# Optimization experiments

Measured on AMD Instinct MI355X. Metric: run time of the kernel, lower is better.

## Reference

```python
import jax, jax.numpy as jnp
import numpy as np
from jax import lax

IMG = 800.0      # image size (square)
STRIDE = 8       # FPN P3 stride
HF = 100; WF = 100; C = 256
A = 3            # anchors per location (aspect ratios 0.5,1,2)
PRE_NMS = 2000   # rpn_pre_nms_top_n_train
POST_NMS = 1000  # rpn_post_nms_top_n_test
NMS_TH = 0.7     # rpn_nms_thresh
POOL = 7; SR = 2 # ROIAlign output size / sampling ratio
NUM_CLASSES = 2
REP = 1024       # TwoMLPHead representation size
BBOX_CLAMP = float(np.log(1000.0 / 16.0))


def make_anchors():
    size = 64.0
    ratios = np.array([0.5, 1.0, 2.0])
    h = size * np.sqrt(ratios); w = size / np.sqrt(ratios)
    base = np.stack([-w / 2, -h / 2, w / 2, h / 2], 1)  # [A,4]
    sy = np.arange(HF) * STRIDE; sx = np.arange(WF) * STRIDE
    yy, xx = np.meshgrid(sy, sx, indexing='ij')
    shifts = np.stack([xx, yy, xx, yy], -1).reshape(-1, 1, 4)  # [H*W,1,4]
    return (shifts + base[None]).reshape(-1, 4).astype(np.float32)  # [H*W*A,4], (H,W,A) order


def conv2d(x, w, b, pad):
    y = lax.conv_general_dilated(x, w, (1, 1), pad, dimension_numbers=('NCHW', 'OIHW', 'NCHW'))
    return y + b[None, :, None, None]


def decode(deltas, anchors):
    wa = anchors[:, 2] - anchors[:, 0]; ha = anchors[:, 3] - anchors[:, 1]
    cxa = anchors[:, 0] + 0.5 * wa; cya = anchors[:, 1] + 0.5 * ha
    dw = jnp.minimum(deltas[:, 2], BBOX_CLAMP)
    dh = jnp.minimum(deltas[:, 3], BBOX_CLAMP)
    cx = deltas[:, 0] * wa + cxa; cy = deltas[:, 1] * ha + cya
    w = jnp.exp(dw) * wa; h = jnp.exp(dh) * ha
    return jnp.stack([cx - 0.5 * w, cy - 0.5 * h, cx + 0.5 * w, cy + 0.5 * h], 1)


def box_iou_one(box, boxes):
    lt = jnp.maximum(box[:2], boxes[:, :2]); rb = jnp.minimum(box[2:], boxes[:, 2:])
    wh = jnp.clip(rb - lt, 0.0)
    inter = wh[:, 0] * wh[:, 1]
    a1 = (box[2] - box[0]) * (box[3] - box[1])
    a2 = (boxes[:, 2] - boxes[:, 0]) * (boxes[:, 3] - boxes[:, 1])
    return inter / (a1 + a2 - inter + 1e-9)


def nms_fixed(boxes, scores, thresh, keep_n):
    order = jnp.argsort(-scores)
    b = boxes[order]; s = scores[order]
    n = b.shape[0]; ar = jnp.arange(n)
    def body(i, alive):
        sup = (box_iou_one(b[i], b) > thresh) & (ar > i) & alive[i]
        return alive & (~sup)
    alive = lax.fori_loop(0, n, body, jnp.ones((n,), bool))
    _, idx = lax.top_k(jnp.where(alive, s, -jnp.inf), keep_n)
    return b[idx]  # [keep_n,4]


def roi_align_one(feat, roi):
    # feat [C,Hf,Wf], roi [4] in image coords (x1,y1,x2,y2)
    Hf, Wf = feat.shape[1], feat.shape[2]
    x1, y1, x2, y2 = roi / STRIDE
    bw = (x2 - x1) / POOL; bh = (y2 - y1) / POOL
    k = (jnp.arange(POOL * SR) + 0.5) / SR  # [S]
    xs = jnp.clip(x1 + bw * k, 0.0, Wf - 1.0)
    ys = jnp.clip(y1 + bh * k, 0.0, Hf - 1.0)
    y0 = jnp.floor(ys); x0 = jnp.floor(xs)
    y0i = y0.astype(jnp.int32); x0i = x0.astype(jnp.int32)
    y1i = jnp.minimum(y0i + 1, Hf - 1); x1i = jnp.minimum(x0i + 1, Wf - 1)
    ly = ys - y0; lx = xs - x0; hy = 1.0 - ly; hx = 1.0 - lx
    v00 = feat[:, y0i[:, None], x0i[None, :]]
    v01 = feat[:, y0i[:, None], x1i[None, :]]
    v10 = feat[:, y1i[:, None], x0i[None, :]]
    v11 = feat[:, y1i[:, None], x1i[None, :]]
    out = ((hy[:, None] * hx[None, :]) * v00 + (hy[:, None] * lx[None, :]) * v01
           + (ly[:, None] * hx[None, :]) * v10 + (ly[:, None] * lx[None, :]) * v11)  # [C,S,S]
    return out.reshape(feat.shape[0], POOL, SR, POOL, SR).mean(axis=(2, 4))  # [C,7,7]


def _forward(features, rpn_conv_w, rpn_conv_b, rpn_cls_w, rpn_cls_b, rpn_bbox_w, rpn_bbox_b,
             fc1_w, fc1_b, fc2_w, fc2_b, cls_w, cls_b, reg_w, reg_b):
    B = features.shape[0]
    t = jax.nn.relu(conv2d(features, rpn_conv_w, rpn_conv_b, 'SAME'))
    obj = conv2d(t, rpn_cls_w, rpn_cls_b, 'VALID').transpose(0, 2, 3, 1).reshape(B, -1)  # (H,W,A)
    dl = (conv2d(t, rpn_bbox_w, rpn_bbox_b, 'VALID')
          .reshape(B, A, 4, HF, WF).transpose(0, 3, 4, 1, 2).reshape(B, -1, 4))
    anchors = jnp.asarray(make_anchors())

    def per_image(feat, o, d):
        s, idx = lax.top_k(o, PRE_NMS)
        boxes = jnp.clip(decode(d[idx], anchors[idx]), 0.0, IMG)
        rois = nms_fixed(boxes, s, NMS_TH, POST_NMS)
        return jax.vmap(lambda r: roi_align_one(feat, r))(rois)  # [K,C,7,7]

    pooled = jax.vmap(per_image)(features, obj, dl)  # [B,K,C,7,7]
    x = pooled.reshape(B, POST_NMS, -1)
    x = jax.nn.relu(x @ fc1_w + fc1_b)
    x = jax.nn.relu(x @ fc2_w + fc2_b)
    return jnp.concatenate([x @ cls_w + cls_b, x @ reg_w + reg_b], axis=-1)  # [B,K,10]


def setup_inputs() -> dict:
    key = jax.random.key(0)
    ks = jax.random.split(key, 8)
    def w(k, shape, s=0.01):
        return jax.random.normal(k, shape, jnp.float32) * s
    return {
        'features': jax.random.normal(ks[0], (2, C, HF, WF), jnp.float32),
        'rpn_conv_w': w(ks[1], (C, C, 3, 3)), 'rpn_conv_b': jnp.zeros((C,), jnp.float32),
        'rpn_cls_w': w(ks[2], (A, C, 1, 1)), 'rpn_cls_b': jnp.zeros((A,), jnp.float32),
        'rpn_bbox_w': w(ks[3], (4 * A, C, 1, 1)), 'rpn_bbox_b': jnp.zeros((4 * A,), jnp.float32),
        'fc1_w': w(ks[4], (C * POOL * POOL, REP)), 'fc1_b': jnp.zeros((REP,), jnp.float32),
        'fc2_w': w(ks[5], (REP, REP)), 'fc2_b': jnp.zeros((REP,), jnp.float32),
        'cls_w': w(ks[6], (REP, NUM_CLASSES)), 'cls_b': jnp.zeros((NUM_CLASSES,), jnp.float32),
        'reg_w': w(ks[7], (REP, 4 * NUM_CLASSES)), 'reg_b': jnp.zeros((4 * NUM_CLASSES,), jnp.float32),
    }


def reference(features, rpn_conv_w, rpn_conv_b, rpn_cls_w, rpn_cls_b, rpn_bbox_w, rpn_bbox_b,
              fc1_w, fc1_b, fc2_w, fc2_b, cls_w, cls_b, reg_w, reg_b):
    return _forward(features, rpn_conv_w, rpn_conv_b, rpn_cls_w, rpn_cls_b, rpn_bbox_w,
                    rpn_bbox_b, fc1_w, fc1_b, fc2_w, fc2_b, cls_w, cls_b, reg_w, reg_b)
```

## Files before the change

### kernel.cpp

```cpp
#include <hip/hip_runtime.h>
#include <hip/hip_bf16.h>
#include <math.h>

#define NPOS 10000
#define NANCH 30000
#define PRE 2000
#define POST 1000
#define RESQ 4096
#define CLAMPD 4.135166556742356
#define FPH 102
#define FPW 132

typedef __attribute__((ext_vector_type(8))) short bf16x8v;
typedef __attribute__((ext_vector_type(4))) float f32x4v;

__device__ __forceinline__ unsigned long long mapu64(double f) {
  unsigned long long b = (unsigned long long)__double_as_longlong(f);
  return (b & 0x8000000000000000ULL) ? ~b : (b | 0x8000000000000000ULL);
}
__device__ __forceinline__ unsigned mapu32(float f) {
  unsigned b = __float_as_uint(f);
  return (b & 0x80000000u) ? ~b : (b | 0x80000000u);
}

__device__ __forceinline__ void async_load16(const void* g, void* l) {
  __builtin_amdgcn_global_load_lds((const __attribute__((address_space(1))) void*)g,
                                   (__attribute__((address_space(3))) void*)l, 16, 0, 0);
}

__global__ void repack_w_k(const float* __restrict__ w, double* __restrict__ wT64r) {
  int tid = blockIdx.x * 256 + threadIdx.x;
  if (tid >= 589824) return;
  int co = tid / 2304;
  int rem = tid % 2304;
  int ci = rem / 9, tap = rem % 9;
  wT64r[((size_t)tap * 256 + ci) * 256 + co] = (double)w[tid];
}

__global__ void wbt_k(const float* __restrict__ w, __hip_bfloat16* __restrict__ wBt) {
  int i = blockIdx.x * 256 + threadIdx.x;
  if (i >= 589824) return;
  int tap = i >> 16;
  int co = (i >> 8) & 255;
  int ci = i & 255;
  wBt[i] = __float2bfloat16(w[(co * 256 + ci) * 9 + tap]);
}

__global__ void transpose_feat_k(const float* __restrict__ feat, float* __restrict__ featT) {
  __shared__ float tile[32][33];
  int b = blockIdx.z;
  int c0 = blockIdx.y * 32;
  int p0 = blockIdx.x * 32;
  int tx = threadIdx.x & 31, ty = threadIdx.x >> 5;
  for (int r = 0; r < 4; ++r) {
    int c = c0 + ty + r * 8, p = p0 + tx;
    tile[ty + r * 8][tx] = (p < NPOS) ? feat[((size_t)b * 256 + c) * NPOS + p] : 0.f;
  }
  __syncthreads();
  for (int r = 0; r < 4; ++r) {
    int p = p0 + ty + r * 8, c = c0 + tx;
    if (p < NPOS) featT[((size_t)b * NPOS + p) * 256 + c] = tile[tx][ty + r * 8];
  }
}

__global__ void fpad_zero_k(__hip_bfloat16* __restrict__ f) {
  size_t i = (size_t)blockIdx.x * 256 + threadIdx.x;
  uint4 z = {0, 0, 0, 0};
  ((uint4*)f)[i] = z;
}

__global__ void fpad_fill_k(const float* __restrict__ feat, __hip_bfloat16* __restrict__ fpadB) {
  __shared__ float tile[32][33];
  int b = blockIdx.z;
  int c0 = blockIdx.y * 32;
  int p0 = blockIdx.x * 32;
  int tx = threadIdx.x & 31, ty = threadIdx.x >> 5;
  for (int r = 0; r < 4; ++r) {
    int c = c0 + ty + r * 8, p = p0 + tx;
    tile[ty + r * 8][tx] = (p < NPOS) ? feat[((size_t)b * 256 + c) * NPOS + p] : 0.f;
  }
  __syncthreads();
  for (int r = 0; r < 4; ++r) {
    int p = p0 + ty + r * 8, c = c0 + tx;
    if (p < NPOS) {
      int y = p / 100, x = p % 100;
      fpadB[(((size_t)b * FPH + y + 1) * FPW + (x + 1)) * 256 + c] =
          __float2bfloat16(tile[tx][ty + r * 8]);
    }
  }
}

__global__ __launch_bounds__(256) void conv_mfma_k(const __hip_bfloat16* __restrict__ fpadB,
                                                   const __hip_bfloat16* __restrict__ wBt,
                                                   const float* __restrict__ bias,
                                                   float* __restrict__ t32) {
  __shared__ __hip_bfloat16 As[128 * 64];
  __shared__ __hip_bfloat16 Bs[128 * 64];
  const int t = threadIdx.x;
  const int wv = t >> 6;
  const int lane = t & 63;
  const int lr = lane & 15, lg = lane >> 4;
  const int wr = wv >> 1, wc = wv & 1;
  const int co0 = blockIdx.x * 128;
  const int mt = blockIdx.y;
  const int img = mt / 100;
  const int rem = mt % 100;
  const int y0 = (rem / 4) * 4, x0 = (rem % 4) * 32;

  f32x4v acc[4][4];
#pragma unroll
  for (int i = 0; i < 4; ++i)
#pragma unroll
    for (int j = 0; j < 4; ++j)
#pragma unroll
      for (int r = 0; r < 4; ++r) acc[i][j][r] = 0.f;

  int srow[4], sseg[4];
#pragma unroll
  for (int i = 0; i < 4; ++i) {
    int c = i * 256 + t;
    srow[i] = c >> 3;
    sseg[i] = (c & 7) ^ (srow[i] & 7);
  }
  int arow[4], brow[4], sk[2];
#pragma unroll
  for (int ms = 0; ms < 4; ++ms) arow[ms] = (wr * 64 + ms * 16 + lr) * 128;
#pragma unroll
  for (int ns = 0; ns < 4; ++ns) brow[ns] = (wc * 64 + ns * 16 + lr) * 128;
#pragma unroll
  for (int kk = 0; kk < 2; ++kk) sk[kk] = (((kk * 4 + lg) ^ (lr & 7)) * 16);

  for (int chunk = 0; chunk < 36; ++chunk) {
    int tap = chunk >> 2;
    int ci0 = (chunk & 3) * 64;
    int dy = tap / 3, dx = tap % 3;
    __syncthreads();
#pragma unroll
    for (int i = 0; i < 4; ++i) {
      int r = srow[i];
      int py = y0 + (r >> 5) + dy, px = x0 + (r & 31) + dx;
      const __hip_bfloat16* ga =
          fpadB + ((((size_t)img * FPH + py) * FPW + px) << 8) + ci0 + sseg[i] * 8;
      async_load16(ga, (char*)As + ((i * 256 + wv * 64) * 16));
    }
#pragma unroll
    for (int i = 0; i < 4; ++i) {
      int r = srow[i];
      const __hip_bfloat16* gb =
          wBt + ((size_t)(tap * 256 + co0 + r) << 8) + ci0 + sseg[i] * 8;
      async_load16(gb, (char*)Bs + ((i * 256 + wv * 64) * 16));
    }
    __syncthreads();

    bf16x8v af[2][4], bf[2][4];
#pragma unroll
    for (int kk = 0; kk < 2; ++kk) {
#pragma unroll
      for (int ms = 0; ms < 4; ++ms)
        af[kk][ms] = *(const bf16x8v*)((const char*)As + arow[ms] + sk[kk]);
#pragma unroll
      for (int ns = 0; ns < 4; ++ns)
        bf[kk][ns] = *(const bf16x8v*)((const char*)Bs + brow[ns] + sk[kk]);
    }
#pragma unroll
    for (int ms = 0; ms < 4; ++ms)
#pragma unroll
      for (int ns = 0; ns < 4; ++ns) {
        acc[ms][ns] = __builtin_amdgcn_mfma_f32_16x16x32_bf16(af[0][ms], bf[0][ns], acc[ms][ns], 0, 0, 0);
        acc[ms][ns] = __builtin_amdgcn_mfma_f32_16x16x32_bf16(af[1][ms], bf[1][ns], acc[ms][ns], 0, 0, 0);
      }
  }

#pragma unroll
  for (int ms = 0; ms < 4; ++ms) {
    int mbase = wr * 64 + ms * 16 + lg * 4;
#pragma unroll
    for (int ns = 0; ns < 4; ++ns) {
      int gn = co0 + wc * 64 + ns * 16 + lr;
      float bv = bias[gn];
#pragma unroll
      for (int r = 0; r < 4; ++r) {
        int m = mbase + r;
        int y = y0 + (m >> 5), x = x0 + (m & 31);
        if (x < 100)
          t32[((size_t)(img * NPOS + y * 100 + x)) * 256 + gn] = fmaxf(acc[ms][ns][r] + bv, 0.f);
      }
    }
  }
}

__global__ void rpn_obj_k(const float* __restrict__ t32, const float* __restrict__ wcls,
                          const float* __restrict__ bcls, float* __restrict__ obj) {
  __shared__ float wl[3][256];
  int tid = threadIdx.x;
  for (int i = tid; i < 768; i += 256) wl[i / 256][i % 256] = wcls[i];
  __syncthreads();
  int gp = blockIdx.x * 256 + tid;
  if (gp >= 2 * NPOS) return;
  const float* tr = t32 + (size_t)gp * 256;
  float a0 = 0.f, a1 = 0.f, a2 = 0.f;
  for (int c = 0; c < 256; c += 4) {
    float4 v = *(const float4*)&tr[c];
    a0 += v.x * wl[0][c] + v.y * wl[0][c + 1] + v.z * wl[0][c + 2] + v.w * wl[0][c + 3];
    a1 += v.x * wl[1][c] + v.y * wl[1][c + 1] + v.z * wl[1][c + 2] + v.w * wl[1][c + 3];
    a2 += v.x * wl[2][c] + v.y * wl[2][c + 1] + v.z * wl[2][c + 2] + v.w * wl[2][c + 3];
  }
  int b = gp / NPOS, lp = gp % NPOS;
  obj[(size_t)b * NANCH + lp * 3 + 0] = a0 + bcls[0];
  obj[(size_t)b * NANCH + lp * 3 + 1] = a1 + bcls[1];
  obj[(size_t)b * NANCH + lp * 3 + 2] = a2 + bcls[2];
}

__global__ __launch_bounds__(1024) void select_k(const float* __restrict__ obj,
                                                 unsigned* __restrict__ cand,
                                                 int* __restrict__ poslist,
                                                 int* __restrict__ counts, float delta) {
  int b = blockIdx.x;
  __shared__ unsigned hist[16][256];
  __shared__ unsigned posbm[320];
  __shared__ unsigned sh_prefix, sh_rem;
  __shared__ int sh_ac, sh_pc;
  int tid = threadIdx.x;
  int wid = tid >> 6;
  const float* ob = obj + (size_t)b * NANCH;

  if (tid == 0) { sh_prefix = 0; sh_rem = PRE; sh_ac = 0; sh_pc = 0; }
  for (int i = tid; i < 320; i += 1024) posbm[i] = 0;
  for (int shift = 24; shift >= 0; shift -= 8) {
    for (int i = tid; i < 16 * 256; i += 1024) ((unsigned*)hist)[i] = 0;
    __syncthreads();
    unsigned pref = sh_prefix;
    unsigned himask = (shift == 24) ? 0u : (0xFFFFFFFFu << (shift + 8));
    for (int i = tid; i < NANCH; i += 1024) {
      unsigned u = mapu32(ob[i]);
      if ((u & himask) == pref) atomicAdd(&hist[wid][(u >> shift) & 255], 1u);
    }
    __syncthreads();
    if (tid < 256) {
      unsigned s = hist[0][tid];
      for (int w = 1; w < 16; ++w) s += hist[w][tid];
      hist[0][tid] = s;
    }
    __syncthreads();
    if (tid == 0) {
      unsigned rem = sh_rem, pfx = sh_prefix;
      for (int bb = 255; bb >= 0; --bb) {
        unsigned c = hist[0][bb];
        if (rem > c) rem -= c;
        else { pfx |= ((unsigned)bb) << shift; break; }
      }
      sh_prefix = pfx; sh_rem = rem;
    }
    __syncthreads();
  }
  unsigned T = sh_prefix;
  float Tval = __uint_as_float((T & 0x80000000u) ? (T & 0x7FFFFFFFu) : ~T);
  float thr = Tval - delta;
  for (int i = tid; i < NANCH; i += 1024) {
    if (ob[i] >= thr) {
      int p = atomicAdd(&sh_ac, 1);
      if (p < RESQ) cand[(size_t)b * RESQ + p] = (unsigned)i;
      int pos = i / 3;
      atomicOr(&posbm[pos >> 5], 1u << (pos & 31));
    }
  }
  __syncthreads();
  for (int w = tid; w < 313; w += 1024) {
    unsigned word = posbm[w];
    while (word) {
      int bit = __builtin_ctz(word);
      word &= word - 1;
      int q = atomicAdd(&sh_pc, 1);
      if (q < RESQ) poslist[(size_t)b * RESQ + q] = w * 32 + bit;
    }
  }
  __syncthreads();
  if (tid == 0) {
    counts[b * 2 + 0] = min(sh_ac, RESQ);
    counts[b * 2 + 1] = min(sh_pc, RESQ);
  }
}

__global__ __launch_bounds__(256) void rescore_t3_k(const float* __restrict__ featT,
                                                    const double* __restrict__ wT64r,
                                                    const int* __restrict__ poslist,
                                                    const int* __restrict__ counts,
                                                    double* __restrict__ t64p) {
  int z = blockIdx.z;
  int b = z / 3, tg = z % 3;
  int cnt = counts[b * 2 + 1];
  int mbase = blockIdx.y * 64;
  if (mbase >= cnt) return;
  int co0 = blockIdx.x * 64;
  __shared__ double As[32][66];
  __shared__ double Bs[32][66];
  __shared__ int sgy[64], sgx[64];
  int tid = threadIdx.x;
  int tx = tid & 15;
  int ty = tid >> 4;
  if (tid < 64) {
    int q = mbase + tid;
    int pos = poslist[(size_t)b * RESQ + (q < cnt ? q : (cnt - 1))];
    sgy[tid] = pos / 100;
    sgx[tid] = pos % 100;
  }
  __syncthreads();
  const float* fb = featT + (size_t)b * NPOS * 256;

  double acc[4][4] = {};
  int ar = tid >> 2, aq = tid & 3;
  int bk = tid >> 3, bq = tid & 7;

  for (int tt = 0; tt < 3; ++tt) {
    int tap = tg * 3 + tt;
    int dy = tap / 3 - 1, dx = tap % 3 - 1;
    for (int cc = 0; cc < 8; ++cc) {
      int ci0 = cc * 32;
      __syncthreads();
      {
        int gy = sgy[ar] + dy, gx = sgx[ar] + dx;
        float4 v0 = {0.f, 0.f, 0.f, 0.f}, v1 = {0.f, 0.f, 0.f, 0.f};
        if (gy >= 0 && gy < 100 && gx >= 0 && gx < 100) {
          const float* fp = &fb[(size_t)(gy * 100 + gx) * 256 + ci0 + aq * 8];
          v0 = *(const float4*)fp;
          v1 = *(const float4*)(fp + 4);
        }
        As[aq * 8 + 0][ar] = (double)v0.x;
        As[aq * 8 + 1][ar] = (double)v0.y;
        As[aq * 8 + 2][ar] = (double)v0.z;
        As[aq * 8 + 3][ar] = (double)v0.w;
        As[aq * 8 + 4][ar] = (double)v1.x;
        As[aq * 8 + 5][ar] = (double)v1.y;
        As[aq * 8 + 6][ar] = (double)v1.z;
        As[aq * 8 + 7][ar] = (double)v1.w;
      }
      {
        const double* gw = wT64r + ((size_t)(tap * 256 + ci0 + bk)) * 256 + co0 + bq * 8;
#pragma unroll
        for (int i = 0; i < 4; ++i)
          *(double2*)&Bs[bk][bq * 8 + i * 2] = *(const double2*)(gw + i * 2);
      }
      __syncthreads();
#pragma unroll
      for (int kk = 0; kk < 32; ++kk) {
        double2 a01 = *(const double2*)&As[kk][ty * 4];
        double2 a23 = *(const double2*)&As[kk][ty * 4 + 2];
        double b0 = Bs[kk][tx];
        double b1 = Bs[kk][tx + 16];
        double b2 = Bs[kk][tx + 32];
        double b3 = Bs[kk][tx + 48];
        acc[0][0] += a01.x * b0; acc[0][1] += a01.x * b1;
        acc[0][2] += a01.x * b2; acc[0][3] += a01.x * b3;
        acc[1][0] += a01.y * b0; acc[1][1] += a01.y * b1;
        acc[1][2] += a01.y * b2; acc[1][3] += a01.y * b3;
        acc[2][0] += a23.x * b0; acc[2][1] += a23.x * b1;
        acc[2][2] += a23.x * b2; acc[2][3] += a23.x * b3;
        acc[3][0] += a23.y * b0; acc[3][1] += a23.y * b1;
        acc[3][2] += a23.y * b2; acc[3][3] += a23.y * b3;
      }
    }
  }
#pragma unroll
  for (int p = 0; p < 4; ++p) {
    int gp = mbase + ty * 4 + p;
    if (gp >= cnt) continue;
    double* outp = t64p + (((size_t)tg * 2 + b) * RESQ + gp) * 256 + co0;
#pragma unroll
    for (int j = 0; j < 4; ++j) outp[tx + 16 * j] = acc[p][j];
  }
}

__global__ __launch_bounds__(256) void rescore_heads_k(const double* __restrict__ t64p,
                                                       const float* __restrict__ bias,
                                                       const int* __restrict__ poslist,
                                                       const int* __restrict__ counts,
                                                       const float* __restrict__ wcls,
                                                       const float* __restrict__ bcls,
                                                       const float* __restrict__ wbbox,
                                                       const float* __restrict__ bbbox,
                                                       double* __restrict__ obj64,
                                                       double* __restrict__ deltas64) {
  int b = blockIdx.y;
  int cnt = counts[b * 2 + 1];
  int base = blockIdx.x * 16;
  if (base >= cnt) return;
  int tid = threadIdx.x;
  if (tid >= 240) return;
  int pp = tid / 15, j = tid % 15;
  int gp = base + pp;
  if (gp >= cnt) return;
  int pos = poslist[(size_t)b * RESQ + gp];
  const double* p0 = t64p + (((size_t)0 * 2 + b) * RESQ + gp) * 256;
  const double* p1 = t64p + (((size_t)1 * 2 + b) * RESQ + gp) * 256;
  const double* p2 = t64p + (((size_t)2 * 2 + b) * RESQ + gp) * 256;
  const float* wr = (j < 3) ? (wcls + j * 256) : (wbbox + (j - 3) * 256);
  double acc = 0.0;
  for (int c = 0; c < 256; ++c) {
    double tv = fmax(p0[c] + p1[c] + p2[c] + (double)bias[c], 0.0);
    acc += tv * (double)wr[c];
  }
  if (j < 3) {
    obj64[(size_t)b * NANCH + pos * 3 + j] = acc + (double)bcls[j];
  } else {
    int jj = j - 3;
    int a = jj >> 2, kk = jj & 3;
    deltas64[((size_t)b * NANCH + pos * 3 + a) * 4 + kk] = acc + (double)bbbox[jj];
  }
}

__global__ __launch_bounds__(1024) void topk_decode_k(const unsigned* __restrict__ cand,
                                                      const int* __restrict__ counts,
                                                      const double* __restrict__ obj64,
                                                      const double* __restrict__ deltas64,
                                                      double* __restrict__ boxesd,
                                                      float* __restrict__ boxesf) {
  int b = blockIdx.x;
  __shared__ unsigned long long selk[RESQ];
  __shared__ unsigned seli[RESQ];
  int tid = threadIdx.x;
  int acnt = counts[b * 2 + 0];
  for (int s = tid; s < RESQ; s += 1024) {
    if (s < acnt) {
      unsigned idx = cand[(size_t)b * RESQ + s];
      selk[s] = mapu64(obj64[(size_t)b * NANCH + idx]);
      seli[s] = idx;
    } else {
      selk[s] = 0ULL;
      seli[s] = 0xFFFFFFFFu;
    }
  }
  __syncthreads();
  for (unsigned k = 2; k <= RESQ; k <<= 1) {
    for (unsigned j = k >> 1; j > 0; j >>= 1) {
      for (int i = tid; i < RESQ; i += 1024) {
        int l = i ^ (int)j;
        if (l > i) {
          unsigned long long ka = selk[i], kb = selk[l];
          unsigned ia = seli[i], ib = seli[l];
          bool before_lb = (kb > ka) || (kb == ka && ib < ia);
          bool asc = ((i & (int)k) == 0);
          if (asc == before_lb) {
            selk[i] = kb; selk[l] = ka;
            seli[i] = ib; seli[l] = ia;
          }
        }
      }
      __syncthreads();
    }
  }
  const double ratios[3] = {0.5, 1.0, 2.0};
  for (int p = tid; p < PRE; p += 1024) {
    unsigned idx = seli[p];
    int a = (int)(idx % 3u);
    int pos = (int)(idx / 3u);
    int ypix = pos / 100, xpix = pos % 100;
    double sx = (double)(xpix * 8), sy = (double)(ypix * 8);
    double sq = sqrt(ratios[a]);
    double w2 = (64.0 / sq) * 0.5;
    double h2 = (64.0 * sq) * 0.5;
    float x1a = (float)(sx - w2), y1a = (float)(sy - h2);
    float x2a = (float)(sx + w2), y2a = (float)(sy + h2);
    double wa = (double)x2a - (double)x1a;
    double ha = (double)y2a - (double)y1a;
    double cxa = (double)x1a + 0.5 * wa, cya = (double)y1a + 0.5 * ha;
    const double* dd = deltas64 + ((size_t)b * NANCH + idx) * 4;
    double dx = dd[0], dy = dd[1];
    double dw = fmin(dd[2], CLAMPD), dh = fmin(dd[3], CLAMPD);
    double cx = dx * wa + cxa, cy = dy * ha + cya;
    double w = exp(dw) * wa, h = exp(dh) * ha;
    double bx1 = fmin(fmax(cx - 0.5 * w, 0.0), 800.0);
    double by1 = fmin(fmax(cy - 0.5 * h, 0.0), 800.0);
    double bx2 = fmin(fmax(cx + 0.5 * w, 0.0), 800.0);
    double by2 = fmin(fmax(cy + 0.5 * h, 0.0), 800.0);
    double* bo = boxesd + ((size_t)b * PRE + p) * 4;
    bo[0] = bx1; bo[1] = by1; bo[2] = bx2; bo[3] = by2;
    float* bf = boxesf + ((size_t)b * PRE + p) * 4;
    bf[0] = (float)bx1; bf[1] = (float)by1; bf[2] = (float)bx2; bf[3] = (float)by2;
  }
}

__global__ void supmat_k(const double* __restrict__ boxes, unsigned* __restrict__ sup) {
  int b = blockIdx.y;
  int gt = blockIdx.x * 256 + threadIdx.x;
  int i = gt >> 6, w = gt & 63;
  if (i >= PRE) return;
  const double* bb = boxes + (size_t)b * PRE * 4;
  double x1 = bb[i * 4 + 0], y1 = bb[i * 4 + 1], x2 = bb[i * 4 + 2], y2 = bb[i * 4 + 3];
  double a1 = (x2 - x1) * (y2 - y1);
  unsigned m = 0;
  int j0 = w * 32;
  for (int jj = 0; jj < 32; ++jj) {
    int j = j0 + jj;
    if (j >= PRE) break;
    if (j > i) {
      double u1 = bb[j * 4 + 0], v1 = bb[j * 4 + 1], u2 = bb[j * 4 + 2], v2 = bb[j * 4 + 3];
      double ltx = fmax(x1, u1), lty = fmax(y1, v1);
      double rbx = fmin(x2, u2), rby = fmin(y2, v2);
      double ww = fmax(rbx - ltx, 0.0), hh = fmax(rby - lty, 0.0);
      double inter = ww * hh;
      double a2 = (u2 - u1) * (v2 - v1);
      double iou = inter / (a1 + a2 - inter + 1e-9);
      if (iou > 0.7) m |= 1u << jj;
    }
  }
  sup[((size_t)b * 2048 + i) * 64 + w] = m;
}

__global__ void nms_emit_k(const unsigned* __restrict__ sup, const float* __restrict__ boxes,
                           float* __restrict__ rois) {
  int b = blockIdx.x;
  int tid = threadIdx.x;
  __shared__ unsigned buf[2][4096];
  __shared__ unsigned aw_s[64];
  __shared__ unsigned pre[64];
  __shared__ unsigned sh_m;
  const unsigned* sb = sup + (size_t)b * 2048 * 64;

  for (int i = tid; i < 4096; i += 256) buf[0][i] = sb[i];
  __syncthreads();

  unsigned aw = 0;
  if (tid < 64) aw = (tid < 62) ? 0xFFFFFFFFu : (tid == 62 ? 0xFFFFu : 0u);

  for (int c = 0; c < 32; ++c) {
    if (tid >= 64 && c + 1 < 32) {
      for (int i = tid - 64; i < 4096; i += 192) buf[(c + 1) & 1][i] = sb[(size_t)(c + 1) * 4096 + i];
    }
    if (tid < 64) {
      const unsigned* B = buf[c & 1];
      unsigned rlo = B[tid * 64 + 2 * c];
      unsigned rhi = B[tid * 64 + 2 * c + 1];
      unsigned clo = __shfl(aw, 2 * c);
      unsigned chi = __shfl(aw, 2 * c + 1);
      unsigned long long cm = (unsigned long long)clo | ((unsigned long long)chi << 32);
      unsigned long long m = cm;
      while (m) {
        int ii = __builtin_ctzll(m);
        unsigned long long kd = (unsigned long long)__shfl(rlo, ii) |
                                ((unsigned long long)__shfl(rhi, ii) << 32);
        cm &= ~kd;
        m = cm & ~((2ULL << ii) - 1ULL);
      }
      unsigned kill = 0;
      unsigned long long m2 = cm;
      while (m2) {
        int i0 = __builtin_ctzll(m2); m2 &= m2 - 1;
        int i1 = -1, i2 = -1, i3 = -1;
        if (m2) { i1 = __builtin_ctzll(m2); m2 &= m2 - 1; }
        if (m2) { i2 = __builtin_ctzll(m2); m2 &= m2 - 1; }
        if (m2) { i3 = __builtin_ctzll(m2); m2 &= m2 - 1; }
        unsigned k0 = B[i0 * 64 + tid];
        unsigned k1 = (i1 >= 0) ? B[i1 * 64 + tid] : 0u;
        unsigned k2 = (i2 >= 0) ? B[i2 * 64 + tid] : 0u;
        unsigned k3 = (i3 >= 0) ? B[i3 * 64 + tid] : 0u;
        kill |= (k0 | k1) | (k2 | k3);
      }
      aw &= ~kill;
    }
    __syncthreads();
  }
  if (tid < 64) aw_s[tid] = aw;
  __syncthreads();
  if (tid == 0) {
    unsigned m = 0;
    for (int w = 0; w < 64; ++w) { pre[w] = m; m += __popc(aw_s[w]); }
    sh_m = m;
  }
  __syncthreads();
  unsigned m = sh_m;
  for (int i = tid; i < PRE; i += 256) {
    int w = i >> 5;
    unsigned word = aw_s[w];
    unsigned lower = word & ((1u << (i & 31)) - 1u);
    unsigned rank = pre[w] + __popc(lower);
    bool al = (word >> (i & 31)) & 1u;
    unsigned dst;
    if (al) {
      if (rank >= POST) continue;
      dst = rank;
    } else {
      unsigned dpos = m + ((unsigned)i - rank);
      if (dpos >= POST) continue;
      dst = dpos;
    }
    const float4 v = *(const float4*)(boxes + ((size_t)b * PRE + i) * 4);
    *(float4*)(rois + ((size_t)b * POST + dst) * 4) = v;
  }
}

__global__ void roi_align_k(const float* __restrict__ featT, const float* __restrict__ rois,
                            __hip_bfloat16* __restrict__ pooled) {
  __shared__ float slx[14], sly[14];
  __shared__ int sx0[14], sx1[14], sy0[14], sy1[14];
  int tid = threadIdx.x;
  int gro = blockIdx.x;
  int b = gro / POST;
  const float* r = rois + (size_t)gro * 4;
  if (tid < 14) {
    float x1 = r[0] * 0.125f, x2 = r[2] * 0.125f;
    float bw = (x2 - x1) / 7.0f;
    float k = ((float)tid + 0.5f) / 2.0f;
    float xs = fminf(fmaxf(x1 + bw * k, 0.f), 99.f);
    float x0f = floorf(xs);
    int x0i = (int)x0f;
    sx0[tid] = x0i; sx1[tid] = min(x0i + 1, 99); slx[tid] = xs - x0f;
  } else if (tid < 28) {
    int s = tid - 14;
    float y1 = r[1] * 0.125f, y2 = r[3] * 0.125f;
    float bh = (y2 - y1) / 7.0f;
    float k = ((float)s + 0.5f) / 2.0f;
    float ys = fminf(fmaxf(y1 + bh * k, 0.f), 99.f);
    float y0f = floorf(ys);
    int y0i = (int)y0f;
    sy0[s] = y0i; sy1[s] = min(y0i + 1, 99); sly[s] = ys - y0f;
  }
  __syncthreads();
  int c = tid;
  const float* fb = featT + (size_t)b * NPOS * 256 + c;
  __hip_bfloat16* outp = pooled + (size_t)gro * 12544 + (size_t)c * 49;
  for (int ph = 0; ph < 7; ++ph) {
    for (int pw = 0; pw < 7; ++pw) {
      float acc = 0.f;
#pragma unroll
      for (int sy = 0; sy < 2; ++sy) {
        int yi = ph * 2 + sy;
        int y0 = sy0[yi], y1 = sy1[yi];
        float ly = sly[yi], hy = 1.f - ly;
#pragma unroll
        for (int sx = 0; sx < 2; ++sx) {
          int xi = pw * 2 + sx;
          int x0 = sx0[xi], x1 = sx1[xi];
          float lx = slx[xi], hx = 1.f - lx;
          float v00 = fb[(size_t)(y0 * 100 + x0) * 256];
          float v01 = fb[(size_t)(y0 * 100 + x1) * 256];
          float v10 = fb[(size_t)(y1 * 100 + x0) * 256];
          float v11 = fb[(size_t)(y1 * 100 + x1) * 256];
          acc += hy * hx * v00 + hy * lx * v01 + ly * hx * v10 + ly * lx * v11;
        }
      }
      outp[ph * 7 + pw] = __float2bfloat16(acc * 0.25f);
    }
  }
}

__global__ void wt_bf16_k(const float* __restrict__ w, __hip_bfloat16* __restrict__ wt,
                          int K, int N) {
  __shared__ float tile[32][33];
  int k0 = blockIdx.x * 32, n0 = blockIdx.y * 32;
  int tx = threadIdx.x & 31, ty = threadIdx.x >> 5;
  for (int r = 0; r < 4; ++r)
    tile[ty + r * 8][tx] = w[(size_t)(k0 + ty + r * 8) * N + n0 + tx];
  __syncthreads();
  for (int r = 0; r < 4; ++r)
    wt[(size_t)(n0 + ty + r * 8) * K + k0 + tx] = __float2bfloat16(tile[tx][ty + r * 8]);
}

__global__ __launch_bounds__(256) void gemm_bf16_k(const __hip_bfloat16* __restrict__ A,
                                                   const __hip_bfloat16* __restrict__ Bt,
                                                   const float* __restrict__ bias,
                                                   __hip_bfloat16* __restrict__ C,
                                                   int N, int K, int relu) {
  __shared__ __hip_bfloat16 As[128 * 64];
  __shared__ __hip_bfloat16 Bs[128 * 64];
  const int t = threadIdx.x;
  const int w = t >> 6;
  const int lane = t & 63;
  const int lr = lane & 15, lg = lane >> 4;
  const int wr = w >> 1, wc = w & 1;
  const int m0 = blockIdx.y * 128, n0 = blockIdx.x * 128;

  f32x4v acc[4][4];
#pragma unroll
  for (int i = 0; i < 4; ++i)
#pragma unroll
    for (int j = 0; j < 4; ++j)
#pragma unroll
      for (int r = 0; r < 4; ++r) acc[i][j][r] = 0.f;

  int srow[4], soff[4];
#pragma unroll
  for (int i = 0; i < 4; ++i) {
    int c = i * 256 + t;
    int row = c >> 3, ccd = c & 7;
    srow[i] = row;
    soff[i] = (ccd ^ (row & 7)) * 8;
  }
  int arow[4], brow[4], sk[2];
#pragma unroll
  for (int ms = 0; ms < 4; ++ms) arow[ms] = (wr * 64 + ms * 16 + lr) * 128;
#pragma unroll
  for (int ns = 0; ns < 4; ++ns) brow[ns] = (wc * 64 + ns * 16 + lr) * 128;
#pragma unroll
  for (int kk = 0; kk < 2; ++kk) sk[kk] = (((kk * 4 + lg) ^ (lr & 7)) * 16);

  for (int k0 = 0; k0 < K; k0 += 64) {
    __syncthreads();
#pragma unroll
    for (int i = 0; i < 4; ++i) {
      const __hip_bfloat16* ga = A + (size_t)(m0 + srow[i]) * K + k0 + soff[i];
      async_load16(ga, (char*)As + ((i * 256 + w * 64) * 16));
    }
#pragma unroll
    for (int i = 0; i < 4; ++i) {
      const __hip_bfloat16* gb = Bt + (size_t)(n0 + srow[i]) * K + k0 + soff[i];
      async_load16(gb, (char*)Bs + ((i * 256 + w * 64) * 16));
    }
    __syncthreads();

    bf16x8v af[2][4], bf[2][4];
#pragma unroll
    for (int kk = 0; kk < 2; ++kk) {
#pragma unroll
      for (int ms = 0; ms < 4; ++ms)
        af[kk][ms] = *(const bf16x8v*)((const char*)As + arow[ms] + sk[kk]);
#pragma unroll
      for (int ns = 0; ns < 4; ++ns)
        bf[kk][ns] = *(const bf16x8v*)((const char*)Bs + brow[ns] + sk[kk]);
    }
#pragma unroll
    for (int ms = 0; ms < 4; ++ms)
#pragma unroll
      for (int ns = 0; ns < 4; ++ns) {
        acc[ms][ns] = __builtin_amdgcn_mfma_f32_16x16x32_bf16(af[0][ms], bf[0][ns], acc[ms][ns], 0, 0, 0);
        acc[ms][ns] = __builtin_amdgcn_mfma_f32_16x16x32_bf16(af[1][ms], bf[1][ns], acc[ms][ns], 0, 0, 0);
      }
  }

#pragma unroll
  for (int ms = 0; ms < 4; ++ms) {
    int gm = m0 + wr * 64 + ms * 16 + lg * 4;
#pragma unroll
    for (int ns = 0; ns < 4; ++ns) {
      int gn = n0 + wc * 64 + ns * 16 + lr;
      float bv = bias[gn];
#pragma unroll
      for (int r = 0; r < 4; ++r) {
        float v = acc[ms][ns][r] + bv;
        if (relu) v = fmaxf(v, 0.f);
        C[(size_t)(gm + r) * N + gn] = __float2bfloat16(v);
      }
    }
  }
}

__global__ void final_heads_k(const __hip_bfloat16* __restrict__ x2,
                              const float* __restrict__ cls_w, const float* __restrict__ cls_b,
                              const float* __restrict__ reg_w, const float* __restrict__ reg_b,
                              float* __restrict__ out) {
  __shared__ float wl[1024][10];
  int tid = threadIdx.x;
  for (int i = tid; i < 1024 * 10; i += 256) {
    int k = i / 10, n = i % 10;
    wl[k][n] = (n < 2) ? cls_w[k * 2 + n] : reg_w[k * 8 + (n - 2)];
  }
  __syncthreads();
  int gt = blockIdx.x * 256 + tid;
  if (gt >= 2 * POST * 10) return;
  int mg = gt / 10, n = gt % 10;
  const __hip_bfloat16* xr = x2 + (size_t)mg * 1024;
  float acc = 0.f;
  for (int k = 0; k < 1024; ++k) acc += __bfloat162float(xr[k]) * wl[k][n];
  acc += (n < 2) ? cls_b[n] : reg_b[n - 2];
  out[(size_t)mg * 10 + n] = acc;
}

extern "C" void kernel_launch(void* const* d_in, const int* in_sizes, int n_in,
                              void* d_out, int out_size, void* d_ws, size_t ws_size,
                              hipStream_t stream) {
  const float* features   = (const float*)d_in[0];
  const float* rpn_conv_w = (const float*)d_in[1];
  const float* rpn_conv_b = (const float*)d_in[2];
  const float* rpn_cls_w  = (const float*)d_in[3];
  const float* rpn_cls_b  = (const float*)d_in[4];
  const float* rpn_bbox_w = (const float*)d_in[5];
  const float* rpn_bbox_b = (const float*)d_in[6];
  const float* fc1_w = (const float*)d_in[7];
  const float* fc1_b = (const float*)d_in[8];
  const float* fc2_w = (const float*)d_in[9];
  const float* fc2_b = (const float*)d_in[10];
  const float* cls_w = (const float*)d_in[11];
  const float* cls_b = (const float*)d_in[12];
  const float* reg_w = (const float*)d_in[13];
  const float* reg_b = (const float*)d_in[14];
  float* out = (float*)d_out;

  char* ws = (char*)d_ws;
  size_t off = 0;
  auto alloc = [&](size_t bytes) -> void* {
    off = (off + 255) & ~(size_t)255;
    void* p = ws + off;
    off += bytes;
    return p;
  };
  float* featT = (float*)alloc((size_t)2 * NPOS * 256 * 4);
  float* rois  = (float*)alloc((size_t)2 * POST * 4 * 4);
  __hip_bfloat16* w1t = (__hip_bfloat16*)alloc((size_t)1024 * 12544 * 2);
  __hip_bfloat16* w2t = (__hip_bfloat16*)alloc((size_t)1024 * 1024 * 2);
  __hip_bfloat16* x1  = (__hip_bfloat16*)alloc((size_t)2048 * 1024 * 2);
  __hip_bfloat16* x2  = (__hip_bfloat16*)alloc((size_t)2048 * 1024 * 2);
  off = (off + 255) & ~(size_t)255;
  size_t region = off;
  double*   wT64r    = (double*)alloc((size_t)589824 * 8);
  __hip_bfloat16* fpadB = (__hip_bfloat16*)alloc((size_t)2 * FPH * FPW * 256 * 2);
  __hip_bfloat16* wBt   = (__hip_bfloat16*)alloc((size_t)589824 * 2);
  off = (off + 255) & ~(size_t)255;
  size_t uni = off;
  float*  t32  = (float*)(ws + uni);
  float*  objf = (float*)(ws + uni + (((size_t)2 * NPOS * 256 * 4 + 255) & ~(size_t)255));
  double* t64p = (double*)(ws + uni);
  size_t uni_sz = (size_t)3 * 2 * RESQ * 256 * 8;
  off = uni + uni_sz;
  double*   obj64    = (double*)alloc((size_t)2 * NANCH * 8);
  double*   deltas64 = (double*)alloc((size_t)2 * NANCH * 4 * 8);
  double*   boxesd   = (double*)alloc((size_t)2 * PRE * 4 * 8);
  float*    boxesf   = (float*)alloc((size_t)2 * PRE * 4 * 4);
  unsigned* sup      = (unsigned*)alloc((size_t)2 * 2048 * 64 * 4);
  unsigned* cand     = (unsigned*)alloc((size_t)2 * RESQ * 4);
  int*      poslist  = (int*)alloc((size_t)2 * RESQ * 4);
  int*      counts   = (int*)alloc(64);
  __hip_bfloat16* pooled = (__hip_bfloat16*)(ws + region);
  size_t pooled_end = region + (size_t)2048 * 12544 * 2;
  if (off < pooled_end) off = pooled_end;
  (void)ws_size; (void)in_sizes; (void)n_in; (void)out_size;

  repack_w_k<<<2304, 256, 0, stream>>>(rpn_conv_w, wT64r);
  wbt_k<<<2304, 256, 0, stream>>>(rpn_conv_w, wBt);
  transpose_feat_k<<<dim3(313, 8, 2), 256, 0, stream>>>(features, featT);
  fpad_zero_k<<<3366, 256, 0, stream>>>(fpadB);
  fpad_fill_k<<<dim3(313, 8, 2), 256, 0, stream>>>(features, fpadB);
  conv_mfma_k<<<dim3(2, 200), 256, 0, stream>>>(fpadB, wBt, rpn_conv_b, t32);
  rpn_obj_k<<<79, 256, 0, stream>>>(t32, rpn_cls_w, rpn_cls_b, objf);
  select_k<<<2, 1024, 0, stream>>>(objf, cand, poslist, counts, 8e-3f);
  rescore_t3_k<<<dim3(4, RESQ / 64, 6), 256, 0, stream>>>(featT, wT64r, poslist, counts, t64p);
  rescore_heads_k<<<dim3(RESQ / 16, 2), 256, 0, stream>>>(t64p, rpn_conv_b, poslist, counts,
                                                          rpn_cls_w, rpn_cls_b, rpn_bbox_w,
                                                          rpn_bbox_b, obj64, deltas64);
  topk_decode_k<<<2, 1024, 0, stream>>>(cand, counts, obj64, deltas64, boxesd, boxesf);
  supmat_k<<<dim3(512, 2), 256, 0, stream>>>(boxesd, sup);
  nms_emit_k<<<2, 256, 0, stream>>>(sup, boxesf, rois);
  wt_bf16_k<<<dim3(392, 32), 256, 0, stream>>>(fc1_w, w1t, 12544, 1024);
  wt_bf16_k<<<dim3(32, 32), 256, 0, stream>>>(fc2_w, w2t, 1024, 1024);
  roi_align_k<<<2 * POST, 256, 0, stream>>>(featT, rois, pooled);
  gemm_bf16_k<<<dim3(8, 16), 256, 0, stream>>>(pooled, w1t, fc1_b, x1, 1024, 12544, 1);
  gemm_bf16_k<<<dim3(8, 16), 256, 0, stream>>>(x1, w2t, fc2_b, x2, 1024, 1024, 1);
  final_heads_k<<<79, 256, 0, stream>>>(x2, cls_w, cls_b, reg_w, reg_b, out);
}
```

Measured before the change: 1.170 ms.

## Split fc1 GEMM over K with narrower tiles and a reduce kernel

The fc1 GEMM (2048x1024x12544) previously launched only 128 blocks of 128x128 tiles, which underfills a GPU with 256 CUs. It now uses 128x64 tiles and a split-K of 2, giving 512 blocks that write fp32 partial sums. A separate kernel adds the partials, applies bias and ReLU, and converts to bf16. This raises parallelism but adds a 16 MB fp32 partial buffer write and read, plus one extra launch.

```diff
diff --git a/kernel.cpp b/kernel.cpp
--- a/kernel.cpp
+++ b/kernel.cpp
@@ -741,6 +741,112 @@
       }
     }
   }
+}
+
+#define FC1K 12544
+#define FC1KS 2
+#define FC1KSEG (FC1K / FC1KS)
+__global__ __launch_bounds__(256) void gemm_part_k(const __hip_bfloat16* __restrict__ A,
+                                                   const __hip_bfloat16* __restrict__ Bt,
+                                                   float* __restrict__ part) {
+  __shared__ __hip_bfloat16 As[128 * 64];
+  __shared__ __hip_bfloat16 Bs[64 * 64];
+  const int t = threadIdx.x;
+  const int w = t >> 6;
+  const int lane = t & 63;
+  const int lr = lane & 15, lg = lane >> 4;
+  const int wr = w >> 1, wc = w & 1;
+  const int m0 = blockIdx.y * 128, n0 = blockIdx.x * 64;
+  const int ks = blockIdx.z;
+  const int kbase = ks * FC1KSEG;
+
+  f32x4v acc[4][2];
+#pragma unroll
+  for (int i = 0; i < 4; ++i)
+#pragma unroll
+    for (int j = 0; j < 2; ++j)
+#pragma unroll
+      for (int r = 0; r < 4; ++r) acc[i][j][r] = 0.f;
+
+  int srow[4], soff[4];
+#pragma unroll
+  for (int i = 0; i < 4; ++i) {
+    int c = i * 256 + t;
+    int row = c >> 3, ccd = c & 7;
+    srow[i] = row;
+    soff[i] = (ccd ^ (row & 7)) * 8;
+  }
+  int arow[4], brow[2], sk[2];
+#pragma unroll
+  for (int ms = 0; ms < 4; ++ms) arow[ms] = (wr * 64 + ms * 16 + lr) * 128;
+#pragma unroll
+  for (int ns = 0; ns < 2; ++ns) brow[ns] = (wc * 32 + ns * 16 + lr) * 128;
+#pragma unroll
+  for (int kk = 0; kk < 2; ++kk) sk[kk] = (((kk * 4 + lg) ^ (lr & 7)) * 16);
+
+  for (int k0 = 0; k0 < FC1KSEG; k0 += 64) {
+    __syncthreads();
+#pragma unroll
+    for (int i = 0; i < 4; ++i) {
+      const __hip_bfloat16* ga = A + (size_t)(m0 + srow[i]) * FC1K + kbase + k0 + soff[i];
+      async_load16(ga, (char*)As + ((i * 256 + w * 64) * 16));
+    }
+#pragma unroll
+    for (int i = 0; i < 2; ++i) {
+      const __hip_bfloat16* gb = Bt + (size_t)(n0 + srow[i]) * FC1K + kbase + k0 + soff[i];
+      async_load16(gb, (char*)Bs + ((i * 256 + w * 64) * 16));
+    }
+    __syncthreads();
+
+    bf16x8v af[2][4], bf[2][2];
+#pragma unroll
+    for (int kk = 0; kk < 2; ++kk) {
+#pragma unroll
+      for (int ms = 0; ms < 4; ++ms)
+        af[kk][ms] = *(const bf16x8v*)((const char*)As + arow[ms] + sk[kk]);
+#pragma unroll
+      for (int ns = 0; ns < 2; ++ns)
+        bf[kk][ns] = *(const bf16x8v*)((const char*)Bs + brow[ns] + sk[kk]);
+    }
+#pragma unroll
+    for (int ms = 0; ms < 4; ++ms)
+#pragma unroll
+      for (int ns = 0; ns < 2; ++ns) {
+        acc[ms][ns] = __builtin_amdgcn_mfma_f32_16x16x32_bf16(af[0][ms], bf[0][ns], acc[ms][ns], 0, 0, 0);
+        acc[ms][ns] = __builtin_amdgcn_mfma_f32_16x16x32_bf16(af[1][ms], bf[1][ns], acc[ms][ns], 0, 0, 0);
+      }
+  }
+
+  float* pb = part + (size_t)ks * 2048 * 1024;
+#pragma unroll
+  for (int ms = 0; ms < 4; ++ms) {
+    int gm = m0 + wr * 64 + ms * 16 + lg * 4;
+#pragma unroll
+    for (int ns = 0; ns < 2; ++ns) {
+      int gn = n0 + wc * 32 + ns * 16 + lr;
+#pragma unroll
+      for (int r = 0; r < 4; ++r)
+        pb[(size_t)(gm + r) * 1024 + gn] = acc[ms][ns][r];
+    }
+  }
+}
+
+__global__ void reduce_bias_relu_k(const float* __restrict__ part, const float* __restrict__ bias,
+                                   __hip_bfloat16* __restrict__ x1) {
+  int i4 = blockIdx.x * 256 + threadIdx.x;
+  if (i4 >= 524288) return;
+  const float4 a = ((const float4*)part)[i4];
+  const float4 b = ((const float4*)part)[524288 + i4];
+  const float4 bv = ((const float4*)bias)[i4 & 255];
+  float v0 = fmaxf(a.x + b.x + bv.x, 0.f);
+  float v1 = fmaxf(a.y + b.y + bv.y, 0.f);
+  float v2 = fmaxf(a.z + b.z + bv.z, 0.f);
+  float v3 = fmaxf(a.w + b.w + bv.w, 0.f);
+  __hip_bfloat16* o = x1 + (size_t)i4 * 4;
+  o[0] = __float2bfloat16(v0);
+  o[1] = __float2bfloat16(v1);
+  o[2] = __float2bfloat16(v2);
+  o[3] = __float2bfloat16(v3);
 }
 
 __global__ void final_heads_k(const __hip_bfloat16* __restrict__ x2,
@@ -819,8 +925,10 @@
   int*      poslist  = (int*)alloc((size_t)2 * RESQ * 4);
   int*      counts   = (int*)alloc(64);
   __hip_bfloat16* pooled = (__hip_bfloat16*)(ws + region);
-  size_t pooled_end = region + (size_t)2048 * 12544 * 2;
-  if (off < pooled_end) off = pooled_end;
+  size_t pooled_sz = (size_t)2048 * 12544 * 2;
+  float* fc1part = (float*)(ws + region + ((pooled_sz + 255) & ~(size_t)255));
+  size_t part_end = region + ((pooled_sz + 255) & ~(size_t)255) + (size_t)FC1KS * 2048 * 1024 * 4;
+  if (off < part_end) off = part_end;
   (void)ws_size; (void)in_sizes; (void)n_in; (void)out_size;
 
   repack_w_k<<<2304, 256, 0, stream>>>(rpn_conv_w, wT64r);
@@ -841,7 +949,8 @@
   wt_bf16_k<<<dim3(392, 32), 256, 0, stream>>>(fc1_w, w1t, 12544, 1024);
   wt_bf16_k<<<dim3(32, 32), 256, 0, stream>>>(fc2_w, w2t, 1024, 1024);
   roi_align_k<<<2 * POST, 256, 0, stream>>>(featT, rois, pooled);
-  gemm_bf16_k<<<dim3(8, 16), 256, 0, stream>>>(pooled, w1t, fc1_b, x1, 1024, 12544, 1);
+  gemm_part_k<<<dim3(16, 16, FC1KS), 256, 0, stream>>>(pooled, w1t, fc1part);
+  reduce_bias_relu_k<<<2048, 256, 0, stream>>>(fc1part, fc1_b, x1);
   gemm_bf16_k<<<dim3(8, 16), 256, 0, stream>>>(x1, w2t, fc2_b, x2, 1024, 1024, 1);
   final_heads_k<<<79, 256, 0, stream>>>(x2, cls_w, cls_b, reg_w, reg_b, out);
 }
```

Result: faster. 1.033 ms (-11.7%).
